# Kernel tuning notes

Measured on AMD Instinct MI355X. Metric: run time of the kernel, lower is better.

## Reference

```python
import jax, jax.numpy as jnp
import numpy as np
import math

ROPE_THETA = 10000.0

def apply_rope(t, pos, theta):
    # t: [b, h, s, d_k] with d_k even; pos: [b, s] int
    d_k = t.shape[-1]
    inv_freq = theta ** (-jnp.arange(0, d_k, 2, dtype=jnp.float32) / d_k)  # [d_k/2]
    angles = pos.astype(jnp.float32)[..., None] * inv_freq  # [b, s, d_k/2]
    cos = jnp.cos(angles)[:, None, :, :]  # [b, 1, s, d_k/2]
    sin = jnp.sin(angles)[:, None, :, :]
    t_even = t[..., 0::2]
    t_odd = t[..., 1::2]
    out_even = cos * t_even - sin * t_odd
    out_odd = sin * t_even + cos * t_odd
    # interleave back: [..., d_k/2, 2] -> [..., d_k]
    return jnp.stack([out_even, out_odd], axis=-1).reshape(t.shape)

def setup_inputs() -> dict:
    key = jax.random.key(0)
    k1, k2, k3, k4, k5 = jax.random.split(key, 5)
    b, s, d_model = 2, 2048, 1024
    std = math.sqrt(2.0 / (2 * d_model))
    return {
        "x": jax.random.normal(k1, (b, s, d_model), dtype=jnp.float32),
        "token_positions": jnp.broadcast_to(jnp.arange(s, dtype=jnp.int32), (b, s)),
        "W_Q": jax.random.normal(k2, (d_model, d_model), dtype=jnp.float32) * std,
        "W_K": jax.random.normal(k3, (d_model, d_model), dtype=jnp.float32) * std,
        "W_V": jax.random.normal(k4, (d_model, d_model), dtype=jnp.float32) * std,
        "W_O": jax.random.normal(k5, (d_model, d_model), dtype=jnp.float32) * std,
    }

def reference(x, token_positions, W_Q, W_K, W_V, W_O):
    b, s, d_model = x.shape
    n_heads = 16
    d_k = d_model // n_heads

    def proj(W):
        # x @ W^T then split heads: [b, s, d_model] -> [b, h, s, d_k]
        y = jnp.einsum('bsd,ed->bse', x, W)
        return y.reshape(b, s, n_heads, d_k).transpose(0, 2, 1, 3)

    Q = apply_rope(proj(W_Q), token_positions, ROPE_THETA)
    K = apply_rope(proj(W_K), token_positions, ROPE_THETA)
    V = proj(W_V)

    scores = jnp.einsum('bhqd,bhkd->bhqk', Q, K) / math.sqrt(d_k)
    causal = jnp.tril(jnp.ones((s, s), dtype=bool))  # True = keep
    scores = jnp.where(causal, scores, -jnp.inf)
    attn = jax.nn.softmax(scores, axis=-1)
    out = jnp.einsum('bhqk,bhkd->bhqd', attn, V)
    out = out.transpose(0, 2, 1, 3).reshape(b, s, d_model)  # merge heads
    return jnp.einsum('bse,de->bsd', out, W_O)
```

## Files before the change

### kernel.cpp

```cpp
#include <hip/hip_runtime.h>
#include <hip/hip_bf16.h>

typedef __attribute__((ext_vector_type(8))) short short8;
typedef __attribute__((ext_vector_type(4))) short short4v;
typedef __attribute__((ext_vector_type(4))) float f32x4;

#define LN10000_DIV32 0.2878231366242558f
#define SCALE_Q_LOG2E 0.18033688011112042f
#define EXP_BIAS 12.0f

__device__ __forceinline__ unsigned short f2bf(float f){
  union { float fv; unsigned u; } a; a.fv = f;
  return (unsigned short)((a.u + 0x7fffu + ((a.u >> 16) & 1u)) >> 16);
}

__global__ __launch_bounds__(256) void convert_all(
    const float* __restrict__ x, const float* __restrict__ wq,
    const float* __restrict__ wk, const float* __restrict__ wv,
    const float* __restrict__ wo, unsigned short* __restrict__ dst,
    float2* __restrict__ tab)
{
  size_t t = (size_t)blockIdx.x * 256 + threadIdx.x;
  if (t < 65536UL){
    const int s = (int)(t >> 5), ip = (int)(t & 31);
    float invf = __expf(-(float)ip * LN10000_DIV32);
    float ang = (float)s * invf;
    tab[t] = make_float2(__cosf(ang), __sinf(ang));
  }
  size_t e = t * 8;
  const float* src; size_t off;
  if (e < 4194304UL)      { src = x;  off = e; }
  else if (e < 5242880UL) { src = wq; off = e - 4194304UL; }
  else if (e < 6291456UL) { src = wk; off = e - 5242880UL; }
  else if (e < 7340032UL) { src = wv; off = e - 6291456UL; }
  else                    { src = wo; off = e - 7340032UL; }
  float4 f0 = *(const float4*)(src + off);
  float4 f1 = *(const float4*)(src + off + 4);
  short8 o;
  o[0] = (short)f2bf(f0.x); o[1] = (short)f2bf(f0.y);
  o[2] = (short)f2bf(f0.z); o[3] = (short)f2bf(f0.w);
  o[4] = (short)f2bf(f1.x); o[5] = (short)f2bf(f1.y);
  o[6] = (short)f2bf(f1.z); o[7] = (short)f2bf(f1.w);
  *(short8*)(dst + e) = o;
}

__global__ __launch_bounds__(256, 2) void gemm_qkv(
    const unsigned short* __restrict__ Xb, const unsigned short* __restrict__ Wb,
    const int* __restrict__ positions, const float2* __restrict__ tab,
    unsigned short* __restrict__ Qb, unsigned short* __restrict__ Kb,
    unsigned short* __restrict__ Vtb)
{
  __shared__ __align__(16) unsigned short As[2*8192];
  __shared__ __align__(16) unsigned short Bs[2*12288];
  f32x4 acc[4][6] = {};
  const int tid = threadIdx.x, lane = tid & 63, w = tid >> 6;
  const int wm = w >> 1, wn = w & 1;
  const int fr = lane & 15, fq = lane >> 4;
  const int id  = blockIdx.x;
  const int xcd = id & 7;
  const int lid = id >> 3;
  const int m0 = (lid & 31) * 128;
  const int n0 = (xcd*2 + (lid >> 5)) * 192;
  const bool have_next = true;

#define STAGE_ALL(kt, buf) do {                                                     \
    _Pragma("unroll")                                                               \
    for (int i_ = 0; i_ < 4; ++i_){                             \
      const int c_ = i_*256 + tid;                                                  \
      const int row_ = c_ >> 3, cd_ = c_ & 7;                                       \
      const int sc_ = (cd_ ^ (row_ & 7)) << 3;                                      \
      const unsigned short* ga_ = Xb + (size_t)(m0 + row_) * 1024 + (kt)*64 + sc_;  \
      __builtin_amdgcn_global_load_lds((const __attribute__((address_space(1))) void*)ga_, \
          (__attribute__((address_space(3))) void*)(As + (buf)*8192 + c_*8), 16, 0, 0);    \
    }                                                                               \
    _Pragma("unroll")                                                               \
    for (int i_ = 0; i_ < 6; ++i_){                             \
      const int c_ = i_*256 + tid;                                                  \
      const int row_ = c_ >> 3, cd_ = c_ & 7;                                       \
      const int sc_ = (cd_ ^ (row_ & 7)) << 3;                                      \
      const unsigned short* gb_ = Wb + (size_t)(n0 + row_) * 1024 + (kt)*64 + sc_;  \
      __builtin_amdgcn_global_load_lds((const __attribute__((address_space(1))) void*)gb_, \
          (__attribute__((address_space(3))) void*)(Bs + (buf)*12288 + c_*8), 16, 0, 0);   \
    }                                                                               \
  } while(0)

  STAGE_ALL(0, 0);

  const int row_a0 = wm*64 + fr;
  const int row_b0 = wn*96 + fr;

  for (int t = 0; t < 16; ++t){
    const int cur = t & 1;
    asm volatile("s_waitcnt vmcnt(0)" ::: "memory");
    __builtin_amdgcn_s_barrier();
    asm volatile("" ::: "memory");
    if (t + 1 < 16) STAGE_ALL(t + 1, cur ^ 1);
    const unsigned short* as = As + cur*8192;
    const unsigned short* bs = Bs + cur*12288;
    short8 af[4], bfv[6];

#define LDA(mf_, kh_) do { \
      const int row_ = row_a0 + (mf_)*16; \
      const int c_ = ((kh_)*4 + fq) ^ (row_ & 7); \
      af[mf_] = *(const short8*)(as + row_*64 + c_*8); } while(0)
#define LDB(nf_, kh_) do { \
      const int row_ = row_b0 + (nf_)*16; \
      const int c_ = ((kh_)*4 + fq) ^ (row_ & 7); \
      bfv[nf_] = *(const short8*)(bs + row_*64 + c_*8); } while(0)

    LDA(0,0); LDA(1,0); LDA(2,0); LDA(3,0);
    LDB(0,0); LDB(1,0); LDB(2,0); LDB(3,0); LDB(4,0); LDB(5,0);
    __builtin_amdgcn_s_setprio(1);
    #pragma unroll
    for (int mf = 0; mf < 4; ++mf)
      #pragma unroll
      for (int nf = 0; nf < 6; ++nf)
        acc[mf][nf] = __builtin_amdgcn_mfma_f32_16x16x32_bf16(af[mf], bfv[nf], acc[mf][nf], 0, 0, 0);
    __builtin_amdgcn_s_setprio(0);

    LDA(0,1); LDA(1,1); LDA(2,1); LDA(3,1);
    LDB(0,1); LDB(1,1); LDB(2,1); LDB(3,1); LDB(4,1); LDB(5,1);
    __builtin_amdgcn_s_setprio(1);
    #pragma unroll
    for (int mf = 0; mf < 4; ++mf)
      #pragma unroll
      for (int nf = 0; nf < 6; ++nf)
        acc[mf][nf] = __builtin_amdgcn_mfma_f32_16x16x32_bf16(af[mf], bfv[nf], acc[mf][nf], 0, 0, 0);
    __builtin_amdgcn_s_setprio(0);
    asm volatile("" ::: "memory");
#undef LDA
#undef LDB
  }
#undef STAGE_ALL

  #pragma unroll
  for (int mf = 0; mf < 4; ++mf){
    int pm[4];
    #pragma unroll
    for (int r = 0; r < 4; ++r){
      const int m = m0 + wm*64 + mf*16 + fq*4 + r;
      pm[r] = positions[m] & 2047;
    }
    const int mbase = m0 + wm*64 + mf*16 + fq*4;
    const int b = mbase >> 11;
    const int s0 = mbase & 2047;
    #pragma unroll
    for (int nf = 0; nf < 6; ++nf){
      const int n = n0 + wn*96 + nf*16 + fr;
      const int seg = n >> 10;
      const int h = (n & 1023) >> 6, d = n & 63;
      const size_t bh = (size_t)b * 16 + h;
      if (seg == 2){
        short4v pack;
        #pragma unroll
        for (int r = 0; r < 4; ++r)
          pack[r] = (short)f2bf(acc[mf][nf][r]);
        *(short4v*)&Vtb[(bh*64 + d)*2048 + s0] = pack;
      } else {
        const int ip = d >> 1;
        #pragma unroll
        for (int r = 0; r < 4; ++r){
          float v = acc[mf][nf][r];
          float pv = __shfl_xor(v, 1);
          const float2 cs = tab[(pm[r] << 5) + ip];
          float outv = (d & 1) ? (cs.x * v + cs.y * pv)
                               : (cs.x * v - cs.y * pv);
          if (seg == 0) outv *= SCALE_Q_LOG2E;
          const unsigned short ob = f2bf(outv);
          const int s = s0 + r;
          if (seg == 0) Qb[(bh*2048 + s)*64 + d] = ob;
          else          Kb[(bh*2048 + s)*64 + d] = ob;
        }
      }
    }
  }
}

__global__ __launch_bounds__(256) void attn_kernel(
    const unsigned short* __restrict__ Qb, const unsigned short* __restrict__ Kb,
    const unsigned short* __restrict__ Vtb, unsigned short* __restrict__ Ob)
{
  __shared__ __align__(16) unsigned short Ks[2][4096];
  __shared__ __align__(16) unsigned short Vs[2][4096];
  __shared__ __align__(16) unsigned short Plds[4][16][64];

  const int tid = threadIdx.x, lane = tid & 63, w = tid >> 6;
  const int fr = lane & 15, fq = lane >> 4;

  const int i = blockIdx.x;
  const int bh = (i & 7) | (((i >> 3) & 3) << 3);
  const int tile = 31 - (i >> 5);
  const int b = bh >> 4, h = bh & 15;
  const int q0 = tile * 64 + w * 16;
  const size_t qk_base = (size_t)bh * 2048 * 64;
  const unsigned short* kbase = Kb + qk_base;
  const unsigned short* vbase = Vtb + (size_t)bh * 64 * 2048;

  const unsigned short* qp = Qb + qk_base + (size_t)(q0 + fr) * 64 + fq * 8;
  short8 aq0 = *(const short8*)qp;
  short8 aq1 = *(const short8*)(qp + 32);

  f32x4 accO[4] = {};
  float lrun = 0.f;
  const int qrow = q0 + fr;
  const int nt = tile + 1;
  const int sw3 = (fr & 7) << 2;

#define STAGE_KV(t_, buf_) do {                                                     \
    const int kv0_ = (t_) * 64;                                                     \
    _Pragma("unroll")                                                               \
    for (int ii_ = 0; ii_ < 2; ++ii_){                                              \
      const int chunk_ = ii_ * 256 + tid;                                           \
      const int row_ = chunk_ >> 3, cd_ = chunk_ & 7;                               \
      const int sc_ = (cd_ ^ (row_ & 7)) << 3;                                      \
      const unsigned short* ksrc_ = kbase + (size_t)(kv0_ + row_) * 64 + sc_;       \
      const unsigned short* vsrc_ = vbase + (size_t)row_ * 2048 + kv0_ + sc_;       \
      __builtin_amdgcn_global_load_lds((const __attribute__((address_space(1))) void*)ksrc_, \
          (__attribute__((address_space(3))) void*)(&Ks[buf_][0] + chunk_*8), 16, 0, 0);     \
      __builtin_amdgcn_global_load_lds((const __attribute__((address_space(1))) void*)vsrc_, \
          (__attribute__((address_space(3))) void*)(&Vs[buf_][0] + chunk_*8), 16, 0, 0);     \
    }                                                                               \
  } while(0)

  STAGE_KV(0, 0);
  for (int t = 0; t < nt; ++t){
    const int cur = t & 1;
    const int kv0 = t * 64;
    if (t + 1 < nt){
      STAGE_KV(t + 1, cur ^ 1);
      asm volatile("s_waitcnt vmcnt(4)" ::: "memory");
    } else {
      asm volatile("s_waitcnt vmcnt(0)" ::: "memory");
    }
    __builtin_amdgcn_s_barrier();
    asm volatile("" ::: "memory");
    const unsigned short* ks = &Ks[cur][0];
    const unsigned short* vs = &Vs[cur][0];

    f32x4 sT[4];
    #pragma unroll
    for (int kf = 0; kf < 4; ++kf){
      const int row = kf*16 + fr;
      const int swr = row & 7;
      short8 k0 = *(const short8*)(ks + row*64 + ((fq ^ swr) << 3));
      short8 k1 = *(const short8*)(ks + row*64 + (((4 + fq) ^ swr) << 3));
      f32x4 s = {0.f, 0.f, 0.f, 0.f};
      s = __builtin_amdgcn_mfma_f32_16x16x32_bf16(k0, aq0, s, 0, 0, 0);
      s = __builtin_amdgcn_mfma_f32_16x16x32_bf16(k1, aq1, s, 0, 0, 0);
      sT[kf] = s;
    }
    if (t == nt - 1){
      #pragma unroll
      for (int kf = 0; kf < 4; ++kf)
        #pragma unroll
        for (int r = 0; r < 4; ++r){
          const int kvcol = kv0 + kf*16 + fq*4 + r;
          if (kvcol > qrow) sT[kf][r] = -1e30f;
        }
    }
    float p[4][4];
    float rs = 0.f;
    #pragma unroll
    for (int kf = 0; kf < 4; ++kf)
      #pragma unroll
      for (int r = 0; r < 4; ++r){
        p[kf][r] = __builtin_amdgcn_exp2f(sT[kf][r] - EXP_BIAS);
        rs += p[kf][r];
      }
    rs += __shfl_xor(rs, 16);
    rs += __shfl_xor(rs, 32);
    lrun += rs;
    unsigned* prow = (unsigned*)&Plds[w][fr][0];
    #pragma unroll
    for (int kf = 0; kf < 4; ++kf)
      #pragma unroll
      for (int jj = 0; jj < 2; ++jj){
        unsigned pk;
        asm("v_cvt_pk_bf16_f32 %0, %1, %2" : "=v"(pk) : "v"(p[kf][2*jj]), "v"(p[kf][2*jj+1]));
        prow[(kf*8 + fq*2 + jj) ^ sw3] = pk;
      }
    asm volatile("s_waitcnt lgkmcnt(0)" ::: "memory");
    const unsigned* crow = (const unsigned*)&Plds[w][fr][0];
    short8 ap0 = *(const short8*)&crow[(fq*4) ^ sw3];
    short8 ap1 = *(const short8*)&crow[(16 + fq*4) ^ sw3];
    __builtin_amdgcn_s_setprio(1);
    #pragma unroll
    for (int dblk = 0; dblk < 4; ++dblk){
      const int d = dblk*16 + fr;
      const int swd = d & 7;
      short8 bv0 = *(const short8*)(vs + d*64 + ((fq ^ swd) << 3));
      short8 bv1 = *(const short8*)(vs + d*64 + (((4 + fq) ^ swd) << 3));
      accO[dblk] = __builtin_amdgcn_mfma_f32_16x16x32_bf16(ap0, bv0, accO[dblk], 0, 0, 0);
      accO[dblk] = __builtin_amdgcn_mfma_f32_16x16x32_bf16(ap1, bv1, accO[dblk], 0, 0, 0);
    }
    __builtin_amdgcn_s_setprio(0);
    asm volatile("" ::: "memory");
    __builtin_amdgcn_s_barrier();
  }
#undef STAGE_KV
  float lq[4];
  #pragma unroll
  for (int r = 0; r < 4; ++r)
    lq[r] = __shfl(lrun, fq*4 + r);
  #pragma unroll
  for (int dblk = 0; dblk < 4; ++dblk)
    #pragma unroll
    for (int r = 0; r < 4; ++r){
      const int s = q0 + fq*4 + r;
      const float o = accO[dblk][r] / lq[r];
      Ob[((size_t)b*2048 + s)*1024 + h*64 + dblk*16 + fr] = f2bf(o);
    }
}

__global__ __launch_bounds__(256) void gemm_out(
    const unsigned short* __restrict__ Obf, const unsigned short* __restrict__ Wb,
    float* __restrict__ out)
{
  __shared__ __align__(16) unsigned short As[3*4096];
  __shared__ __align__(16) unsigned short Bs[3*2048];
  f32x4 acc[4][2] = {};
  const int tid = threadIdx.x, lane = tid & 63, w = tid >> 6;
  const int wm = w >> 1, wn = w & 1;
  const int fr = lane & 15, fq = lane >> 4;
  const int id  = blockIdx.x;
  const int xcd = id & 7;
  const int lid = id >> 3;
  const int m0 = (xcd*4 + (lid & 3)) * 128;
  const int n0 = (lid >> 2) * 64;
  const int ph = ((fq ^ ((fr + (fr >> 2)) & 3))) * 8;

#define STAGEO(kt, buf) do {                                                        \
    _Pragma("unroll")                                                               \
    for (int i_ = 0; i_ < 2; ++i_){                                                 \
      const int c_ = i_*256 + tid;                                                  \
      const int row_ = c_ >> 2, cd_ = c_ & 3;                                       \
      const int sc_ = ((cd_ ^ ((row_ + (row_ >> 2)) & 3))) << 3;                    \
      const unsigned short* ga_ = Obf + (size_t)(m0 + row_) * 1024 + (kt)*32 + sc_; \
      __builtin_amdgcn_global_load_lds((const __attribute__((address_space(1))) void*)ga_, \
          (__attribute__((address_space(3))) void*)(As + (buf)*4096 + c_*8), 16, 0, 0);    \
    }                                                                               \
    {                                                                               \
      const int c_ = tid;                                                           \
      const int row_ = c_ >> 2, cd_ = c_ & 3;                                       \
      const int sc_ = ((cd_ ^ ((row_ + (row_ >> 2)) & 3))) << 3;                    \
      const unsigned short* gb_ = Wb + (size_t)(n0 + row_) * 1024 + (kt)*32 + sc_;  \
      __builtin_amdgcn_global_load_lds((const __attribute__((address_space(1))) void*)gb_, \
          (__attribute__((address_space(3))) void*)(Bs + (buf)*2048 + c_*8), 16, 0, 0);    \
    }                                                                               \
  } while(0)

  STAGEO(0, 0);
  STAGEO(1, 1);
  for (int t = 0; t < 32; ++t){
    const int cur = t % 3;
    if (t + 2 < 32) STAGEO(t + 2, (t + 2) % 3);
    if (t < 30)       asm volatile("s_waitcnt vmcnt(6)" ::: "memory");
    else if (t == 30) asm volatile("s_waitcnt vmcnt(3)" ::: "memory");
    else              asm volatile("s_waitcnt vmcnt(0)" ::: "memory");
    __builtin_amdgcn_s_barrier();
    asm volatile("" ::: "memory");
    const unsigned short* as = As + cur*4096;
    const unsigned short* bs = Bs + cur*2048;
    short8 af[4], bfv[2];
    #pragma unroll
    for (int mf = 0; mf < 4; ++mf)
      af[mf] = *(const short8*)(as + (wm*64 + mf*16 + fr) * 32 + ph);
    #pragma unroll
    for (int nf = 0; nf < 2; ++nf)
      bfv[nf] = *(const short8*)(bs + (wn*32 + nf*16 + fr) * 32 + ph);
    #pragma unroll
    for (int mf = 0; mf < 4; ++mf)
      #pragma unroll
      for (int nf = 0; nf < 2; ++nf)
        acc[mf][nf] = __builtin_amdgcn_mfma_f32_16x16x32_bf16(af[mf], bfv[nf], acc[mf][nf], 0, 0, 0);
    asm volatile("" ::: "memory");
    __builtin_amdgcn_s_barrier();
  }
#undef STAGEO

  #pragma unroll
  for (int mf = 0; mf < 4; ++mf)
    #pragma unroll
    for (int nf = 0; nf < 2; ++nf){
      const int n = n0 + wn*32 + nf*16 + fr;
      #pragma unroll
      for (int r = 0; r < 4; ++r){
        const int m = m0 + wm*64 + mf*16 + fq*4 + r;
        out[(size_t)m * 1024 + n] = acc[mf][nf][r];
      }
    }
}

extern "C" void kernel_launch(void* const* d_in, const int* in_sizes, int n_in,
                              void* d_out, int out_size, void* d_ws, size_t ws_size,
                              hipStream_t stream) {
  const float* x  = (const float*)d_in[0];
  const int* pos  = (const int*)d_in[1];
  const float* wq = (const float*)d_in[2];
  const float* wk = (const float*)d_in[3];
  const float* wv = (const float*)d_in[4];
  const float* wo = (const float*)d_in[5];
  float* out = (float*)d_out;

  unsigned short* ws = (unsigned short*)d_ws;
  unsigned short* Xb   = ws;
  unsigned short* Wqkv = ws + 4194304UL;
  unsigned short* Wo   = ws + 7340032UL;
  unsigned short* Qb   = ws + 8388608UL;
  unsigned short* Kb   = ws + 12582912UL;
  unsigned short* Vt   = ws + 16777216UL;
  unsigned short* Ob   = ws + 20971520UL;
  float2* tab          = (float2*)(ws + 25165824UL);

  convert_all<<<4096, 256, 0, stream>>>(x, wq, wk, wv, wo, ws, tab);

  gemm_qkv<<<512, 256, 0, stream>>>(Xb, Wqkv, pos, tab, Qb, Kb, Vt);

  attn_kernel<<<1024, 256, 0, stream>>>(Qb, Kb, Vt, Ob);

  gemm_out<<<512, 256, 0, stream>>>(Ob, Wo, out);
}
```

Baseline: 104.6 us.

## Use two waves per attention block with 32 query rows each

Attention blocks shrink from four waves of 16 query rows to two waves of 32 query rows. Each wave reuses its K and V fragments read from LDS across two query sub-tiles, so LDS reads per MFMA are halved. Each thread now issues twice as many KV staging loads, and the vmcnt wait is raised to match. Register pressure per wave grows and each block has fewer waves to hide latency, though more blocks can be resident per CU.

```diff
diff --git a/kernel.cpp b/kernel.cpp
--- a/kernel.cpp
+++ b/kernel.cpp
@@ -61,7 +61,6 @@
   const int lid = id >> 3;
   const int m0 = (lid & 31) * 128;
   const int n0 = (xcd*2 + (lid >> 5)) * 192;
-  const bool have_next = true;
 
 #define STAGE_ALL(kt, buf) do {                                                     \
     _Pragma("unroll")                                                               \
@@ -176,13 +175,13 @@
   }
 }
 
-__global__ __launch_bounds__(256) void attn_kernel(
+__global__ __launch_bounds__(128) void attn_kernel(
     const unsigned short* __restrict__ Qb, const unsigned short* __restrict__ Kb,
     const unsigned short* __restrict__ Vtb, unsigned short* __restrict__ Ob)
 {
   __shared__ __align__(16) unsigned short Ks[2][4096];
   __shared__ __align__(16) unsigned short Vs[2][4096];
-  __shared__ __align__(16) unsigned short Plds[4][16][64];
+  __shared__ __align__(16) unsigned short Plds[2][32][64];
 
   const int tid = threadIdx.x, lane = tid & 63, w = tid >> 6;
   const int fr = lane & 15, fq = lane >> 4;
@@ -191,26 +190,29 @@
   const int bh = (i & 7) | (((i >> 3) & 3) << 3);
   const int tile = 31 - (i >> 5);
   const int b = bh >> 4, h = bh & 15;
-  const int q0 = tile * 64 + w * 16;
+  const int q0 = tile * 64 + w * 32;
   const size_t qk_base = (size_t)bh * 2048 * 64;
   const unsigned short* kbase = Kb + qk_base;
   const unsigned short* vbase = Vtb + (size_t)bh * 64 * 2048;
 
-  const unsigned short* qp = Qb + qk_base + (size_t)(q0 + fr) * 64 + fq * 8;
-  short8 aq0 = *(const short8*)qp;
-  short8 aq1 = *(const short8*)(qp + 32);
-
-  f32x4 accO[4] = {};
-  float lrun = 0.f;
-  const int qrow = q0 + fr;
+  short8 aq[2][2];
+  #pragma unroll
+  for (int qh = 0; qh < 2; ++qh){
+    const unsigned short* qp = Qb + qk_base + (size_t)(q0 + qh*16 + fr) * 64 + fq * 8;
+    aq[qh][0] = *(const short8*)qp;
+    aq[qh][1] = *(const short8*)(qp + 32);
+  }
+
+  f32x4 accO[2][4] = {};
+  float lrun[2] = {0.f, 0.f};
   const int nt = tile + 1;
   const int sw3 = (fr & 7) << 2;
 
 #define STAGE_KV(t_, buf_) do {                                                     \
     const int kv0_ = (t_) * 64;                                                     \
     _Pragma("unroll")                                                               \
-    for (int ii_ = 0; ii_ < 2; ++ii_){                                              \
-      const int chunk_ = ii_ * 256 + tid;                                           \
+    for (int ii_ = 0; ii_ < 4; ++ii_){                                              \
+      const int chunk_ = ii_ * 128 + tid;                      \
       const int row_ = chunk_ >> 3, cd_ = chunk_ & 7;                               \
       const int sc_ = (cd_ ^ (row_ & 7)) << 3;                                      \
       const unsigned short* ksrc_ = kbase + (size_t)(kv0_ + row_) * 64 + sc_;       \
@@ -228,7 +230,7 @@
     const int kv0 = t * 64;
     if (t + 1 < nt){
       STAGE_KV(t + 1, cur ^ 1);
-      asm volatile("s_waitcnt vmcnt(4)" ::: "memory");
+      asm volatile("s_waitcnt vmcnt(8)" ::: "memory");
     } else {
       asm volatile("s_waitcnt vmcnt(0)" ::: "memory");
     }
@@ -237,52 +239,66 @@
     const unsigned short* ks = &Ks[cur][0];
     const unsigned short* vs = &Vs[cur][0];
 
-    f32x4 sT[4];
+    f32x4 sT[4][2];
     #pragma unroll
     for (int kf = 0; kf < 4; ++kf){
       const int row = kf*16 + fr;
       const int swr = row & 7;
       short8 k0 = *(const short8*)(ks + row*64 + ((fq ^ swr) << 3));
       short8 k1 = *(const short8*)(ks + row*64 + (((4 + fq) ^ swr) << 3));
-      f32x4 s = {0.f, 0.f, 0.f, 0.f};
-      s = __builtin_amdgcn_mfma_f32_16x16x32_bf16(k0, aq0, s, 0, 0, 0);
-      s = __builtin_amdgcn_mfma_f32_16x16x32_bf16(k1, aq1, s, 0, 0, 0);
-      sT[kf] = s;
+      #pragma unroll
+      for (int qh = 0; qh < 2; ++qh){
+        f32x4 s = {0.f, 0.f, 0.f, 0.f};
+        s = __builtin_amdgcn_mfma_f32_16x16x32_bf16(k0, aq[qh][0], s, 0, 0, 0);
+        s = __builtin_amdgcn_mfma_f32_16x16x32_bf16(k1, aq[qh][1], s, 0, 0, 0);
+        sT[kf][qh] = s;
+      }
     }
     if (t == nt - 1){
+      #pragma unroll
+      for (int qh = 0; qh < 2; ++qh){
+        const int qrow = q0 + qh*16 + fr;
+        #pragma unroll
+        for (int kf = 0; kf < 4; ++kf)
+          #pragma unroll
+          for (int r = 0; r < 4; ++r){
+            const int kvcol = kv0 + kf*16 + fq*4 + r;
+            if (kvcol > qrow) sT[kf][qh][r] = -1e30f;
+          }
+      }
+    }
+    #pragma unroll
+    for (int qh = 0; qh < 2; ++qh){
+      float p[4][4];
+      float rs = 0.f;
       #pragma unroll
       for (int kf = 0; kf < 4; ++kf)
         #pragma unroll
         for (int r = 0; r < 4; ++r){
-          const int kvcol = kv0 + kf*16 + fq*4 + r;
-          if (kvcol > qrow) sT[kf][r] = -1e30f;
+          p[kf][r] = __builtin_amdgcn_exp2f(sT[kf][qh][r] - EXP_BIAS);
+          rs += p[kf][r];
         }
-    }
-    float p[4][4];
-    float rs = 0.f;
-    #pragma unroll
-    for (int kf = 0; kf < 4; ++kf)
-      #pragma unroll
-      for (int r = 0; r < 4; ++r){
-        p[kf][r] = __builtin_amdgcn_exp2f(sT[kf][r] - EXP_BIAS);
-        rs += p[kf][r];
-      }
-    rs += __shfl_xor(rs, 16);
-    rs += __shfl_xor(rs, 32);
-    lrun += rs;
-    unsigned* prow = (unsigned*)&Plds[w][fr][0];
-    #pragma unroll
-    for (int kf = 0; kf < 4; ++kf)
-      #pragma unroll
-      for (int jj = 0; jj < 2; ++jj){
-        unsigned pk;
-        asm("v_cvt_pk_bf16_f32 %0, %1, %2" : "=v"(pk) : "v"(p[kf][2*jj]), "v"(p[kf][2*jj+1]));
-        prow[(kf*8 + fq*2 + jj) ^ sw3] = pk;
-      }
+      rs += __shfl_xor(rs, 16);
+      rs += __shfl_xor(rs, 32);
+      lrun[qh] += rs;
+      unsigned* prow = (unsigned*)&Plds[w][qh*16 + fr][0];
+      #pragma unroll
+      for (int kf = 0; kf < 4; ++kf)
+        #pragma unroll
+        for (int jj = 0; jj < 2; ++jj){
+          unsigned pk;
+          asm("v_cvt_pk_bf16_f32 %0, %1, %2" : "=v"(pk) : "v"(p[kf][2*jj]), "v"(p[kf][2*jj+1]));
+          prow[(kf*8 + fq*2 + jj) ^ sw3] = pk;
+        }
+    }
     asm volatile("s_waitcnt lgkmcnt(0)" ::: "memory");
-    const unsigned* crow = (const unsigned*)&Plds[w][fr][0];
-    short8 ap0 = *(const short8*)&crow[(fq*4) ^ sw3];
-    short8 ap1 = *(const short8*)&crow[(16 + fq*4) ^ sw3];
+    short8 ap[2][2];
+    #pragma unroll
+    for (int qh = 0; qh < 2; ++qh){
+      const unsigned* crow = (const unsigned*)&Plds[w][qh*16 + fr][0];
+      ap[qh][0] = *(const short8*)&crow[(fq*4) ^ sw3];
+      ap[qh][1] = *(const short8*)&crow[(16 + fq*4) ^ sw3];
+    }
     __builtin_amdgcn_s_setprio(1);
     #pragma unroll
     for (int dblk = 0; dblk < 4; ++dblk){
@@ -290,26 +306,32 @@
       const int swd = d & 7;
       short8 bv0 = *(const short8*)(vs + d*64 + ((fq ^ swd) << 3));
       short8 bv1 = *(const short8*)(vs + d*64 + (((4 + fq) ^ swd) << 3));
-      accO[dblk] = __builtin_amdgcn_mfma_f32_16x16x32_bf16(ap0, bv0, accO[dblk], 0, 0, 0);
-      accO[dblk] = __builtin_amdgcn_mfma_f32_16x16x32_bf16(ap1, bv1, accO[dblk], 0, 0, 0);
+      #pragma unroll
+      for (int qh = 0; qh < 2; ++qh){
+        accO[qh][dblk] = __builtin_amdgcn_mfma_f32_16x16x32_bf16(ap[qh][0], bv0, accO[qh][dblk], 0, 0, 0);
+        accO[qh][dblk] = __builtin_amdgcn_mfma_f32_16x16x32_bf16(ap[qh][1], bv1, accO[qh][dblk], 0, 0, 0);
+      }
     }
     __builtin_amdgcn_s_setprio(0);
     asm volatile("" ::: "memory");
     __builtin_amdgcn_s_barrier();
   }
 #undef STAGE_KV
-  float lq[4];
   #pragma unroll
-  for (int r = 0; r < 4; ++r)
-    lq[r] = __shfl(lrun, fq*4 + r);
-  #pragma unroll
-  for (int dblk = 0; dblk < 4; ++dblk)
-    #pragma unroll
-    for (int r = 0; r < 4; ++r){
-      const int s = q0 + fq*4 + r;
-      const float o = accO[dblk][r] / lq[r];
-      Ob[((size_t)b*2048 + s)*1024 + h*64 + dblk*16 + fr] = f2bf(o);
-    }
+  for (int qh = 0; qh < 2; ++qh){
+    float lq[4];
+    #pragma unroll
+    for (int r = 0; r < 4; ++r)
+      lq[r] = __shfl(lrun[qh], fq*4 + r);
+    #pragma unroll
+    for (int dblk = 0; dblk < 4; ++dblk)
+      #pragma unroll
+      for (int r = 0; r < 4; ++r){
+        const int s = q0 + qh*16 + fq*4 + r;
+        const float o = accO[qh][dblk][r] / lq[r];
+        Ob[((size_t)b*2048 + s)*1024 + h*64 + dblk*16 + fr] = f2bf(o);
+      }
+  }
 }
 
 __global__ __launch_bounds__(256) void gemm_out(
@@ -416,7 +438,7 @@
 
   gemm_qkv<<<512, 256, 0, stream>>>(Xb, Wqkv, pos, tab, Qb, Kb, Vt);
 
-  attn_kernel<<<1024, 256, 0, stream>>>(Qb, Kb, Vt, Ob);
+  attn_kernel<<<1024, 128, 0, stream>>>(Qb, Kb, Vt, Ob);
 
   gemm_out<<<512, 256, 0, stream>>>(Ob, Wo, out);
 }
```

After: 112.0 us. 7.1% more time.
